# Performance work log

Hardware: AMD Instinct MI355X
Metric: run time of the kernel (lower is better)

## Reference

```python
import jax, jax.numpy as jnp
import numpy as np

ITER_N = 5  # Newton-Schulz iterations (SqrtmLayer(cov, 5))


def covpool(x):
    # x: [B, C, M]. MPNCOV CovpoolLayer: x @ I_hat @ x^T with
    # I_hat = (1/M)(I - J/M), a projector, so cov = xc @ xc^T / M.
    M = x.shape[-1]
    xc = x - x.mean(axis=-1, keepdims=True)
    return jnp.einsum('bcm,bdm->bcd', xc, xc) / M


def sqrtm_ns(A, iter_n=ITER_N):
    # MPNCOV SqrtmLayer: trace-normalized Newton-Schulz matrix square root.
    C = A.shape[-1]
    I = jnp.eye(C, dtype=A.dtype)
    normA = jnp.trace(A, axis1=-2, axis2=-1)[:, None, None]  # [B,1,1]
    Y = A / normA
    Z = jnp.broadcast_to(I, A.shape)
    for i in range(iter_n):
        T = 0.5 * (3.0 * I - Z @ Y)
        Y_new = Y @ T
        if i < iter_n - 1:
            Z = T @ Z
        Y = Y_new
    return Y * jnp.sqrt(normA)


def setup_inputs() -> dict:
    key = jax.random.key(0)
    k1, k2, k3 = jax.random.split(key, 3)
    B, C, H, W = 32, 256, 64, 64
    r = 8
    x = jax.random.normal(k1, (B, C, H, W), dtype=jnp.float32)
    w1 = jax.random.normal(k2, (C // r, C), dtype=jnp.float32) * 0.05
    b1 = jnp.zeros((C // r,), dtype=jnp.float32)
    w2 = jax.random.normal(k3, (C, C // r), dtype=jnp.float32) * 0.05
    b2 = jnp.zeros((C,), dtype=jnp.float32)
    return {'x': x, 'w1': w1, 'b1': b1, 'w2': w2, 'b2': b2}


def reference(x, w1, b1, w2, b2):
    B, C, h, w = x.shape
    # h, w < 1000 => x_sub = x (no center crop)
    xf = x.reshape(B, C, h * w)
    cov = covpool(xf)                      # [B, C, C]
    cov_sqrt = sqrtm_ns(cov, ITER_N)       # [B, C, C]
    v = cov_sqrt.mean(axis=1)              # mean over dim 1 -> [B, C]
    # 1x1 convs on a 1x1 map == dense layers
    hdn = jax.nn.relu(jnp.einsum('oc,bc->bo', w1, v) + b1)
    a = jax.nn.sigmoid(jnp.einsum('oc,bc->bo', w2, hdn) + b2)  # [B, C]
    return a[:, :, None, None] * x
```

## Files before the change

kernel.cpp:

```cpp
#include <hip/hip_runtime.h>
#include <hip/hip_bf16.h>

typedef unsigned int uint32;
using short8 = __attribute__((ext_vector_type(8))) short;
using f32x4  = __attribute__((ext_vector_type(4))) float;

#define B_ 32
#define C_ 256
#define M_ 4096

__device__ inline ushort f2bf(float f) {
  uint32 u = __builtin_bit_cast(uint32, f);
  u += 0x7FFFu + ((u >> 16) & 1u);
  return (ushort)(u >> 16);
}

__global__ __launch_bounds__(256)
void covpool_kernel(const float* __restrict__ x,
                    float* __restrict__ p0, float* __restrict__ p1,
                    float* __restrict__ p2, float* __restrict__ p3,
                    float* __restrict__ rs) {
  const int bid0 = blockIdx.x;
  const int bid  = (bid0 & 7) * 64 + (bid0 >> 3);
  const int b    = bid >> 4;
  const int tile = (bid >> 2) & 3;
  const int s    = bid & 3;
  const int rb   = (tile >> 1) * 128;
  const int cb   = (tile & 1) * 128;
  const int kb   = s * 1024;
  float* P = (s == 0) ? p0 : (s == 1) ? p1 : (s == 2) ? p2 : p3;

  const float* Xr = x + (size_t)b * C_ * M_ + (size_t)rb * M_;
  const float* Xc = x + (size_t)b * C_ * M_ + (size_t)cb * M_;

  __shared__ ushort As[128 * 64];
  __shared__ ushort Bs[128 * 64];

  const int t    = threadIdx.x;
  const int lane = t & 63;
  const int wid  = t >> 6;
  const int wr   = wid >> 1, wc = wid & 1;
  const int r0   = t >> 3;
  const int c8   = t & 7;

  float sA[4] = {0.f, 0.f, 0.f, 0.f};
  f32x4 acc[4][4];
#pragma unroll
  for (int m = 0; m < 4; ++m)
#pragma unroll
    for (int n = 0; n < 4; ++n) acc[m][n] = f32x4{0.f, 0.f, 0.f, 0.f};

  for (int k0 = kb; k0 < kb + 1024; k0 += 64) {
    __syncthreads();
#pragma unroll
    for (int i = 0; i < 4; ++i) {
      const int row = r0 + 32 * i;
      const int swz = (c8 * 16) ^ ((row & 7) << 4);
      {
        const float4 a0 = *(const float4*)(Xr + (size_t)row * M_ + k0 + c8 * 8);
        const float4 a1 = *(const float4*)(Xr + (size_t)row * M_ + k0 + c8 * 8 + 4);
        sA[i] += a0.x + a0.y + a0.z + a0.w + a1.x + a1.y + a1.z + a1.w;
        short8 h;
        h[0] = (short)f2bf(a0.x); h[1] = (short)f2bf(a0.y);
        h[2] = (short)f2bf(a0.z); h[3] = (short)f2bf(a0.w);
        h[4] = (short)f2bf(a1.x); h[5] = (short)f2bf(a1.y);
        h[6] = (short)f2bf(a1.z); h[7] = (short)f2bf(a1.w);
        *(short8*)((char*)As + row * 128 + swz) = h;
      }
      {
        const float4 b0 = *(const float4*)(Xc + (size_t)row * M_ + k0 + c8 * 8);
        const float4 b1 = *(const float4*)(Xc + (size_t)row * M_ + k0 + c8 * 8 + 4);
        short8 g;
        g[0] = (short)f2bf(b0.x); g[1] = (short)f2bf(b0.y);
        g[2] = (short)f2bf(b0.z); g[3] = (short)f2bf(b0.w);
        g[4] = (short)f2bf(b1.x); g[5] = (short)f2bf(b1.y);
        g[6] = (short)f2bf(b1.z); g[7] = (short)f2bf(b1.w);
        *(short8*)((char*)Bs + row * 128 + swz) = g;
      }
    }
    __syncthreads();
#pragma unroll
    for (int kk = 0; kk < 2; ++kk) {
      short8 af[4], bfr[4];
      const int slot = kk * 4 + (lane >> 4);
#pragma unroll
      for (int m = 0; m < 4; ++m) {
        const int ar = wr * 64 + m * 16 + (lane & 15);
        af[m] = *(const short8*)((const char*)As + ar * 128 + ((slot * 16) ^ ((ar & 7) << 4)));
      }
#pragma unroll
      for (int n = 0; n < 4; ++n) {
        const int br = wc * 64 + n * 16 + (lane & 15);
        bfr[n] = *(const short8*)((const char*)Bs + br * 128 + ((slot * 16) ^ ((br & 7) << 4)));
      }
#pragma unroll
      for (int m = 0; m < 4; ++m)
#pragma unroll
        for (int n = 0; n < 4; ++n)
          acc[m][n] = __builtin_amdgcn_mfma_f32_16x16x32_bf16(af[m], bfr[n], acc[m][n], 0, 0, 0);
    }
  }

#pragma unroll
  for (int i = 0; i < 4; ++i) {
    float v = sA[i];
    v += __shfl_xor(v, 1); v += __shfl_xor(v, 2); v += __shfl_xor(v, 4);
    if ((lane & 7) == 0) rs[b * 1024 + s * 256 + rb + r0 + 32 * i] = v;
  }

  float* Po = P + ((size_t)b << 16);
#pragma unroll
  for (int m = 0; m < 4; ++m)
#pragma unroll
    for (int n = 0; n < 4; ++n)
#pragma unroll
      for (int r = 0; r < 4; ++r) {
        const int lr = wr * 64 + m * 16 + ((lane >> 4) * 4) + r;
        const int lc = wc * 64 + n * 16 + (lane & 15);
        Po[(size_t)(rb + lr) * C_ + (cb + lc)] = acc[m][n][r];
      }
}

__global__ __launch_bounds__(256)
void reduce_kernel(const float* __restrict__ p0, const float* __restrict__ p1,
                   const float* __restrict__ p2, const float* __restrict__ p3,
                   const float* __restrict__ rs, float* __restrict__ cov) {
  const int idx = blockIdx.x * 256 + threadIdx.x;
  const int b   = idx >> 14;
  const int rem = idx & 16383;
  const int i   = rem >> 6;
  const int j4  = (rem & 63) * 4;
  const float invM = 1.0f / (float)M_;

  const float4 g0 = ((const float4*)p0)[idx];
  const float4 g1 = ((const float4*)p1)[idx];
  const float4 g2 = ((const float4*)p2)[idx];
  const float4 g3 = ((const float4*)p3)[idx];

  const float* rb_ = rs + b * 1024;
  const float mi = (rb_[i] + rb_[256 + i] + rb_[512 + i] + rb_[768 + i]) * invM;
  const float4 s0 = *(const float4*)(rb_ + j4);
  const float4 s1 = *(const float4*)(rb_ + 256 + j4);
  const float4 s2 = *(const float4*)(rb_ + 512 + j4);
  const float4 s3 = *(const float4*)(rb_ + 768 + j4);

  float4 o;
  o.x = (g0.x + g1.x + g2.x + g3.x) * invM - mi * ((s0.x + s1.x + s2.x + s3.x) * invM);
  o.y = (g0.y + g1.y + g2.y + g3.y) * invM - mi * ((s0.y + s1.y + s2.y + s3.y) * invM);
  o.z = (g0.z + g1.z + g2.z + g3.z) * invM - mi * ((s0.z + s1.z + s2.z + s3.z) * invM);
  o.w = (g0.w + g1.w + g2.w + g3.w) * invM - mi * ((s0.w + s1.w + s2.w + s3.w) * invM);
  ((float4*)cov)[idx] = o;
}

__global__ __launch_bounds__(256)
void trace_kernel(const float* __restrict__ cov, float* __restrict__ invn,
                  float* __restrict__ sqrtn) {
  const int b = blockIdx.x;
  const int t = threadIdx.x;
  float v = cov[((size_t)b << 16) + (size_t)t * 257];
#pragma unroll
  for (int o = 32; o > 0; o >>= 1) v += __shfl_xor(v, o);
  __shared__ float wsum[4];
  if ((t & 63) == 0) wsum[t >> 6] = v;
  __syncthreads();
  if (t == 0) {
    const float n = wsum[0] + wsum[1] + wsum[2] + wsum[3];
    invn[b]  = 1.0f / n;
    sqrtn[b] = sqrtf(n);
  }
}

__global__ __launch_bounds__(256)
void prep_kernel(const float* __restrict__ cov, const float* __restrict__ invn,
                 float* __restrict__ Y, float* __restrict__ Z) {
  const int idx = blockIdx.x * 256 + threadIdx.x;
  const int b  = idx >> 14;
  const int w4 = idx & 16383;
  const int i  = w4 >> 6;
  const int j  = (w4 & 63) * 4;
  const float in = invn[b];
  const float4 c = ((const float4*)cov)[idx];
  float4 y = { c.x * in, c.y * in, c.z * in, c.w * in };
  float4 z = { (j + 0 == i ? 1.5f : 0.f) - 0.5f * y.x,
               (j + 1 == i ? 1.5f : 0.f) - 0.5f * y.y,
               (j + 2 == i ? 1.5f : 0.f) - 0.5f * y.z,
               (j + 3 == i ? 1.5f : 0.f) - 0.5f * y.w };
  ((float4*)Y)[idx] = y;
  ((float4*)Z)[idx] = z;
}

#define MODE_T 0
#define MODE_W 1
#define MODE_I0 2

template <int MODE>
__global__ __launch_bounds__(256)
void gemm_ns(const float* __restrict__ A0, const float* __restrict__ A1,
             const float* __restrict__ Bm,
             float* __restrict__ O0, float* __restrict__ O1) {
  int bid = blockIdx.x;
  const float* Aall = A0;
  float* Oall = O0;
  if (MODE == MODE_W && bid >= 512) { bid -= 512; Aall = A1; Oall = O1; }
  const int b    = bid >> 4;
  const int tile = bid & 15;
  const int rb   = (tile >> 2) * 64;
  const int cb   = (tile & 3) * 64;
  const float* Ap = Aall + ((size_t)b << 16) + rb * C_;
  const float* Bp = Bm   + ((size_t)b << 16) + cb * C_;
  float* Op = Oall + ((size_t)b << 16);

  __shared__ ushort As[64 * 64];
  __shared__ ushort Bs[64 * 64];

  const int t    = threadIdx.x;
  const int lane = t & 63;
  const int wid  = t >> 6;
  const int wr   = wid >> 1, wc = wid & 1;
  const int r0   = t >> 3;
  const int c8   = t & 7;

  f32x4 acc[2][2];
#pragma unroll
  for (int m = 0; m < 2; ++m)
#pragma unroll
    for (int n = 0; n < 2; ++n) acc[m][n] = f32x4{0.f, 0.f, 0.f, 0.f};

#pragma unroll 1
  for (int k0 = 0; k0 < C_; k0 += 64) {
    __syncthreads();
#pragma unroll
    for (int i = 0; i < 2; ++i) {
      const int row = r0 + 32 * i;
      const int swz = (c8 * 16) ^ ((row & 7) << 4);
      {
        const float4 a0 = *(const float4*)(Ap + row * C_ + k0 + c8 * 8);
        const float4 a1 = *(const float4*)(Ap + row * C_ + k0 + c8 * 8 + 4);
        short8 h;
        h[0] = (short)f2bf(a0.x); h[1] = (short)f2bf(a0.y);
        h[2] = (short)f2bf(a0.z); h[3] = (short)f2bf(a0.w);
        h[4] = (short)f2bf(a1.x); h[5] = (short)f2bf(a1.y);
        h[6] = (short)f2bf(a1.z); h[7] = (short)f2bf(a1.w);
        *(short8*)((char*)As + row * 128 + swz) = h;
      }
      {
        const float4 b0 = *(const float4*)(Bp + row * C_ + k0 + c8 * 8);
        const float4 b1 = *(const float4*)(Bp + row * C_ + k0 + c8 * 8 + 4);
        short8 g;
        g[0] = (short)f2bf(b0.x); g[1] = (short)f2bf(b0.y);
        g[2] = (short)f2bf(b0.z); g[3] = (short)f2bf(b0.w);
        g[4] = (short)f2bf(b1.x); g[5] = (short)f2bf(b1.y);
        g[6] = (short)f2bf(b1.z); g[7] = (short)f2bf(b1.w);
        *(short8*)((char*)Bs + row * 128 + swz) = g;
      }
    }
    __syncthreads();
#pragma unroll
    for (int kk = 0; kk < 2; ++kk) {
      short8 af[2], bfr[2];
      const int slot = kk * 4 + (lane >> 4);
#pragma unroll
      for (int m = 0; m < 2; ++m) {
        const int ar = wr * 32 + m * 16 + (lane & 15);
        af[m] = *(const short8*)((const char*)As + ar * 128 + ((slot * 16) ^ ((ar & 7) << 4)));
      }
#pragma unroll
      for (int n = 0; n < 2; ++n) {
        const int br = wc * 32 + n * 16 + (lane & 15);
        bfr[n] = *(const short8*)((const char*)Bs + br * 128 + ((slot * 16) ^ ((br & 7) << 4)));
      }
#pragma unroll
      for (int m = 0; m < 2; ++m)
#pragma unroll
        for (int n = 0; n < 2; ++n)
          acc[m][n] = __builtin_amdgcn_mfma_f32_16x16x32_bf16(af[m], bfr[n], acc[m][n], 0, 0, 0);
    }
  }

#pragma unroll
  for (int m = 0; m < 2; ++m)
#pragma unroll
    for (int n = 0; n < 2; ++n)
#pragma unroll
      for (int r = 0; r < 4; ++r) {
        const int lr = wr * 32 + m * 16 + ((lane >> 4) * 4) + r;
        const int lc = wc * 32 + n * 16 + (lane & 15);
        const float v = acc[m][n][r];
        float o;
        if (MODE == MODE_T)       o = (((rb + lr) == (cb + lc)) ? 1.5f : 0.0f) - 0.5f * v;
        else if (MODE == MODE_W)  o = v;
        else         o = 1.5f * Ap[lr * C_ + (cb + lc)] - 0.5f * v;
        Op[(size_t)(rb + lr) * C_ + (cb + lc)] = o;
      }
}

__global__ __launch_bounds__(256)
void final_kernel(const float* __restrict__ Y, const float* __restrict__ T,
                  const float* __restrict__ sqrtn,
                  const float* __restrict__ w1, const float* __restrict__ b1,
                  const float* __restrict__ w2, const float* __restrict__ b2,
                  float* __restrict__ a) {
  const int b = blockIdx.x;
  const int c = threadIdx.x;
  __shared__ float u[C_], vv[C_], h[32];
  const float* Yb = Y + ((size_t)b << 16);
  const float* Tb = T + ((size_t)b << 16);

  float s = 0.f;
  for (int i = 0; i < C_; ++i) s += Yb[(size_t)i * C_ + c];
  u[c] = s * (1.0f / (float)C_);
  __syncthreads();

  float acc = 0.f;
  for (int k = 0; k < C_; ++k) acc += u[k] * Tb[(size_t)k * C_ + c];
  vv[c] = acc * sqrtn[b];
  __syncthreads();

  if (c < 32) {
    float hh = b1[c];
    for (int k = 0; k < C_; ++k) hh += w1[c * C_ + k] * vv[k];
    h[c] = fmaxf(hh, 0.0f);
  }
  __syncthreads();

  float aa = b2[c];
#pragma unroll
  for (int o = 0; o < 32; ++o) aa += w2[c * 32 + o] * h[o];
  a[b * C_ + c] = 1.0f / (1.0f + expf(-aa));
}

__global__ __launch_bounds__(256)
void scale_kernel(const float* __restrict__ x, const float* __restrict__ a,
                  float* __restrict__ out) {
  const int stride = gridDim.x * blockDim.x;
  const int n4 = B_ * C_ * M_ / 4;
  for (int i = blockIdx.x * blockDim.x + threadIdx.x; i < n4; i += stride) {
    const float4 v = ((const float4*)x)[i];
    const float s = a[i >> 10];
    float4 o = { v.x * s, v.y * s, v.z * s, v.w * s };
    ((float4*)out)[i] = o;
  }
}

extern "C" void kernel_launch(void* const* d_in, const int* in_sizes, int n_in,
                              void* d_out, int out_size, void* d_ws, size_t ws_size,
                              hipStream_t stream) {
  const float* x  = (const float*)d_in[0];
  const float* w1 = (const float*)d_in[1];
  const float* b1 = (const float*)d_in[2];
  const float* w2 = (const float*)d_in[3];
  const float* b2 = (const float*)d_in[4];
  float* out = (float*)d_out;

  float* ws = (float*)d_ws;
  const size_t MAT = (size_t)B_ * C_ * C_;
  float* covT = ws;
  float* YA   = ws + 1 * MAT;
  float* YB   = ws + 2 * MAT;
  float* ZA   = ws + 3 * MAT;
  float* ZB   = ws + 4 * MAT;
  float* invn  = ws + 5 * MAT;
  float* sqrtn = invn + 32;
  float* a     = sqrtn + 32;
  float* rs    = a + 32 * 256;

  covpool_kernel<<<512, 256, 0, stream>>>(x, YA, YB, ZA, ZB, rs);
  reduce_kernel<<<2048, 256, 0, stream>>>(YA, YB, ZA, ZB, rs, covT);
  trace_kernel<<<32, 256, 0, stream>>>(covT, invn, sqrtn);
  prep_kernel<<<2048, 256, 0, stream>>>(covT, invn, YA, ZA);

  gemm_ns<MODE_I0><<<512, 256, 0, stream>>>(YA, nullptr, YA, YB, nullptr);
  gemm_ns<MODE_T><<<512, 256, 0, stream>>>(ZA, nullptr, YB, covT, nullptr);
  gemm_ns<MODE_W><<<1024, 256, 0, stream>>>(YB, ZA, covT, YA, ZB);
  gemm_ns<MODE_T><<<512, 256, 0, stream>>>(ZB, nullptr, YA, covT, nullptr);
  gemm_ns<MODE_W><<<1024, 256, 0, stream>>>(YA, ZB, covT, YB, ZA);
  gemm_ns<MODE_T><<<512, 256, 0, stream>>>(ZA, nullptr, YB, covT, nullptr);
  gemm_ns<MODE_W><<<1024, 256, 0, stream>>>(YB, ZA, covT, YA, ZB);
  gemm_ns<MODE_T><<<512, 256, 0, stream>>>(ZB, nullptr, YA, covT, nullptr);

  final_kernel<<<32, 256, 0, stream>>>(YA, covT, sqrtn, w1, b1, w2, b2, a);
  scale_kernel<<<4096, 256, 0, stream>>>(x, a, out);
}
```

Before: 420.5 us.

## Store Newton-Schulz matrices in bf16, use direct-to-LDS loads, restructure covpool

Covpool now has one 1024-thread block per (batch, K-split) that computes the full 256x256 Gram from a single shared tile. This halves the global reads of x, since rows and columns come from the same data. The K split grows to 8 partial buffers, and the reduce and prep kernels are fused into one that writes bf16 Y and Z; the trace is taken directly from the partial diagonals. All Newton-Schulz intermediates are kept in bf16, and the GEMM loads use global_load_lds with swizzled addresses, cutting memory traffic and per-element conversion. The risk is lower precision from rounding intermediates to bf16 between iterations, plus more partial-buffer traffic in the reduce step.

```diff
diff --git a/kernel.cpp b/kernel.cpp
--- a/kernel.cpp
+++ b/kernel.cpp
@@ -3,81 +3,79 @@
 
 typedef unsigned int uint32;
 using short8 = __attribute__((ext_vector_type(8))) short;
+using ushort4_t = __attribute__((ext_vector_type(4))) unsigned short;
 using f32x4  = __attribute__((ext_vector_type(4))) float;
 
 #define B_ 32
 #define C_ 256
 #define M_ 4096
+#define MATF 2097152
+
+#define AS1 __attribute__((address_space(1)))
+#define AS3 __attribute__((address_space(3)))
 
 __device__ inline ushort f2bf(float f) {
   uint32 u = __builtin_bit_cast(uint32, f);
   u += 0x7FFFu + ((u >> 16) & 1u);
   return (ushort)(u >> 16);
 }
-
-__global__ __launch_bounds__(256)
-void covpool_kernel(const float* __restrict__ x,
-                    float* __restrict__ p0, float* __restrict__ p1,
-                    float* __restrict__ p2, float* __restrict__ p3,
+__device__ inline float bf2f(ushort u) {
+  uint32 v = ((uint32)u) << 16;
+  return __builtin_bit_cast(float, v);
+}
+__device__ inline void gl_lds16(const ushort* g, ushort* l) {
+  __builtin_amdgcn_global_load_lds((const AS1 void*)g, (AS3 void*)l, 16, 0, 0);
+}
+
+__global__ __launch_bounds__(1024)
+void covpool_kernel(const float* __restrict__ x, float* __restrict__ parts,
                     float* __restrict__ rs) {
-  const int bid0 = blockIdx.x;
-  const int bid  = (bid0 & 7) * 64 + (bid0 >> 3);
-  const int b    = bid >> 4;
-  const int tile = (bid >> 2) & 3;
-  const int s    = bid & 3;
-  const int rb   = (tile >> 1) * 128;
-  const int cb   = (tile & 1) * 128;
-  const int kb   = s * 1024;
-  float* P = (s == 0) ? p0 : (s == 1) ? p1 : (s == 2) ? p2 : p3;
-
-  const float* Xr = x + (size_t)b * C_ * M_ + (size_t)rb * M_;
-  const float* Xc = x + (size_t)b * C_ * M_ + (size_t)cb * M_;
-
-  __shared__ ushort As[128 * 64];
-  __shared__ ushort Bs[128 * 64];
+  const int bid = blockIdx.x;
+  const int b = bid >> 3, s = bid & 7;
+  const int kb = s * 512;
+  const float* Xb = x + (size_t)b * C_ * M_;
+  float* P = parts + (size_t)s * MATF + ((size_t)b << 16);
+
+  __shared__ ushort As[256 * 64];
 
   const int t    = threadIdx.x;
   const int lane = t & 63;
-  const int wid  = t >> 6;
-  const int wr   = wid >> 1, wc = wid & 1;
-  const int r0   = t >> 3;
-  const int c8   = t & 7;
-
-  float sA[4] = {0.f, 0.f, 0.f, 0.f};
+  const int w    = t >> 6;
+  const int wr   = w >> 2, wc = w & 3;
+  const int row  = t >> 2;
+  const int ch   = t & 3;
+
+  float rsum = 0.f;
   f32x4 acc[4][4];
 #pragma unroll
   for (int m = 0; m < 4; ++m)
 #pragma unroll
     for (int n = 0; n < 4; ++n) acc[m][n] = f32x4{0.f, 0.f, 0.f, 0.f};
 
-  for (int k0 = kb; k0 < kb + 1024; k0 += 64) {
+  const int swzbase = (row & 7) << 4;
+  char* wbase = (char*)As + row * 128;
+
+  for (int k0 = kb; k0 < kb + 512; k0 += 64) {
     __syncthreads();
-#pragma unroll
-    for (int i = 0; i < 4; ++i) {
-      const int row = r0 + 32 * i;
-      const int swz = (c8 * 16) ^ ((row & 7) << 4);
-      {
-        const float4 a0 = *(const float4*)(Xr + (size_t)row * M_ + k0 + c8 * 8);
-        const float4 a1 = *(const float4*)(Xr + (size_t)row * M_ + k0 + c8 * 8 + 4);
-        sA[i] += a0.x + a0.y + a0.z + a0.w + a1.x + a1.y + a1.z + a1.w;
-        short8 h;
-        h[0] = (short)f2bf(a0.x); h[1] = (short)f2bf(a0.y);
-        h[2] = (short)f2bf(a0.z); h[3] = (short)f2bf(a0.w);
-        h[4] = (short)f2bf(a1.x); h[5] = (short)f2bf(a1.y);
-        h[6] = (short)f2bf(a1.z); h[7] = (short)f2bf(a1.w);
-        *(short8*)((char*)As + row * 128 + swz) = h;
-      }
-      {
-        const float4 b0 = *(const float4*)(Xc + (size_t)row * M_ + k0 + c8 * 8);
-        const float4 b1 = *(const float4*)(Xc + (size_t)row * M_ + k0 + c8 * 8 + 4);
-        short8 g;
-        g[0] = (short)f2bf(b0.x); g[1] = (short)f2bf(b0.y);
-        g[2] = (short)f2bf(b0.z); g[3] = (short)f2bf(b0.w);
-        g[4] = (short)f2bf(b1.x); g[5] = (short)f2bf(b1.y);
-        g[6] = (short)f2bf(b1.z); g[7] = (short)f2bf(b1.w);
-        *(short8*)((char*)Bs + row * 128 + swz) = g;
-      }
-    }
+    const float* src = Xb + (size_t)row * M_ + k0 + ch * 16;
+    const float4 v0 = ((const float4*)src)[0];
+    const float4 v1 = ((const float4*)src)[1];
+    const float4 v2 = ((const float4*)src)[2];
+    const float4 v3 = ((const float4*)src)[3];
+    rsum += v0.x + v0.y + v0.z + v0.w + v1.x + v1.y + v1.z + v1.w +
+            v2.x + v2.y + v2.z + v2.w + v3.x + v3.y + v3.z + v3.w;
+    short8 h0, h1;
+    h0[0] = (short)f2bf(v0.x); h0[1] = (short)f2bf(v0.y);
+    h0[2] = (short)f2bf(v0.z); h0[3] = (short)f2bf(v0.w);
+    h0[4] = (short)f2bf(v1.x); h0[5] = (short)f2bf(v1.y);
+    h0[6] = (short)f2bf(v1.z); h0[7] = (short)f2bf(v1.w);
+    h1[0] = (short)f2bf(v2.x); h1[1] = (short)f2bf(v2.y);
+    h1[2] = (short)f2bf(v2.z); h1[3] = (short)f2bf(v2.w);
+    h1[4] = (short)f2bf(v3.x); h1[5] = (short)f2bf(v3.y);
+    h1[6] = (short)f2bf(v3.z); h1[7] = (short)f2bf(v3.w);
+    const int c0 = ch * 2;
+    *(short8*)(wbase + ((c0 * 16) ^ swzbase))       = h0;
+    *(short8*)(wbase + (((c0 + 1) * 16) ^ swzbase)) = h1;
     __syncthreads();
 #pragma unroll
     for (int kk = 0; kk < 2; ++kk) {
@@ -91,7 +89,7 @@
 #pragma unroll
       for (int n = 0; n < 4; ++n) {
         const int br = wc * 64 + n * 16 + (lane & 15);
-        bfr[n] = *(const short8*)((const char*)Bs + br * 128 + ((slot * 16) ^ ((br & 7) << 4)));
+        bfr[n] = *(const short8*)((const char*)As + br * 128 + ((slot * 16) ^ ((br & 7) << 4)));
       }
 #pragma unroll
       for (int m = 0; m < 4; ++m)
@@ -101,14 +99,10 @@
     }
   }
 
-#pragma unroll
-  for (int i = 0; i < 4; ++i) {
-    float v = sA[i];
-    v += __shfl_xor(v, 1); v += __shfl_xor(v, 2); v += __shfl_xor(v, 4);
-    if ((lane & 7) == 0) rs[b * 1024 + s * 256 + rb + r0 + 32 * i] = v;
-  }
-
-  float* Po = P + ((size_t)b << 16);
+  rsum += __shfl_xor(rsum, 1);
+  rsum += __shfl_xor(rsum, 2);
+  if (ch == 0) rs[b * 2048 + s * 256 + row] = rsum;
+
 #pragma unroll
   for (int m = 0; m < 4; ++m)
 #pragma unroll
@@ -117,76 +111,75 @@
       for (int r = 0; r < 4; ++r) {
         const int lr = wr * 64 + m * 16 + ((lane >> 4) * 4) + r;
         const int lc = wc * 64 + n * 16 + (lane & 15);
-        Po[(size_t)(rb + lr) * C_ + (cb + lc)] = acc[m][n][r];
-      }
-}
-
-__global__ __launch_bounds__(256)
-void reduce_kernel(const float* __restrict__ p0, const float* __restrict__ p1,
-                   const float* __restrict__ p2, const float* __restrict__ p3,
-                   const float* __restrict__ rs, float* __restrict__ cov) {
+        P[(size_t)lr * C_ + lc] = acc[m][n][r];
+      }
+}
+
+__global__ __launch_bounds__(256)
+void trace_kernel(const float* __restrict__ parts, const float* __restrict__ rs,
+                  float* __restrict__ invn, float* __restrict__ sqrtn) {
+  const int b = blockIdx.x;
+  const int i = threadIdx.x;
+  const float invM = 1.0f / (float)M_;
+  float d = 0.f, m = 0.f;
+#pragma unroll
+  for (int s = 0; s < 8; ++s) {
+    d += parts[(size_t)s * MATF + ((size_t)b << 16) + (size_t)i * 257];
+    m += rs[b * 2048 + s * 256 + i];
+  }
+  const float mu = m * invM;
+  float v = d * invM - mu * mu;
+#pragma unroll
+  for (int o = 32; o > 0; o >>= 1) v += __shfl_xor(v, o);
+  __shared__ float wsum[4];
+  if ((i & 63) == 0) wsum[i >> 6] = v;
+  __syncthreads();
+  if (i == 0) {
+    const float n = wsum[0] + wsum[1] + wsum[2] + wsum[3];
+    invn[b]  = 1.0f / n;
+    sqrtn[b] = sqrtf(n);
+  }
+}
+
+__global__ __launch_bounds__(256)
+void reduceprep_kernel(const float* __restrict__ parts, const float* __restrict__ rs,
+                       const float* __restrict__ invn,
+                       ushort* __restrict__ Y0, ushort* __restrict__ Z1) {
   const int idx = blockIdx.x * 256 + threadIdx.x;
   const int b   = idx >> 14;
   const int rem = idx & 16383;
   const int i   = rem >> 6;
-  const int j4  = (rem & 63) * 4;
+  const int j   = (rem & 63) * 4;
   const float invM = 1.0f / (float)M_;
-
-  const float4 g0 = ((const float4*)p0)[idx];
-  const float4 g1 = ((const float4*)p1)[idx];
-  const float4 g2 = ((const float4*)p2)[idx];
-  const float4 g3 = ((const float4*)p3)[idx];
-
-  const float* rb_ = rs + b * 1024;
-  const float mi = (rb_[i] + rb_[256 + i] + rb_[512 + i] + rb_[768 + i]) * invM;
-  const float4 s0 = *(const float4*)(rb_ + j4);
-  const float4 s1 = *(const float4*)(rb_ + 256 + j4);
-  const float4 s2 = *(const float4*)(rb_ + 512 + j4);
-  const float4 s3 = *(const float4*)(rb_ + 768 + j4);
-
-  float4 o;
-  o.x = (g0.x + g1.x + g2.x + g3.x) * invM - mi * ((s0.x + s1.x + s2.x + s3.x) * invM);
-  o.y = (g0.y + g1.y + g2.y + g3.y) * invM - mi * ((s0.y + s1.y + s2.y + s3.y) * invM);
-  o.z = (g0.z + g1.z + g2.z + g3.z) * invM - mi * ((s0.z + s1.z + s2.z + s3.z) * invM);
-  o.w = (g0.w + g1.w + g2.w + g3.w) * invM - mi * ((s0.w + s1.w + s2.w + s3.w) * invM);
-  ((float4*)cov)[idx] = o;
-}
-
-__global__ __launch_bounds__(256)
-void trace_kernel(const float* __restrict__ cov, float* __restrict__ invn,
-                  float* __restrict__ sqrtn) {
-  const int b = blockIdx.x;
-  const int t = threadIdx.x;
-  float v = cov[((size_t)b << 16) + (size_t)t * 257];
-#pragma unroll
-  for (int o = 32; o > 0; o >>= 1) v += __shfl_xor(v, o);
-  __shared__ float wsum[4];
-  if ((t & 63) == 0) wsum[t >> 6] = v;
-  __syncthreads();
-  if (t == 0) {
-    const float n = wsum[0] + wsum[1] + wsum[2] + wsum[3];
-    invn[b]  = 1.0f / n;
-    sqrtn[b] = sqrtf(n);
-  }
-}
-
-__global__ __launch_bounds__(256)
-void prep_kernel(const float* __restrict__ cov, const float* __restrict__ invn,
-                 float* __restrict__ Y, float* __restrict__ Z) {
-  const int idx = blockIdx.x * 256 + threadIdx.x;
-  const int b  = idx >> 14;
-  const int w4 = idx & 16383;
-  const int i  = w4 >> 6;
-  const int j  = (w4 & 63) * 4;
+  const float4* p4 = (const float4*)parts;
+
+  float4 g = {0.f, 0.f, 0.f, 0.f};
+  float  mi = 0.f;
+  float4 mj = {0.f, 0.f, 0.f, 0.f};
+#pragma unroll
+  for (int s = 0; s < 8; ++s) {
+    const float4 gs = p4[(size_t)s * (MATF / 4) + idx];
+    g.x += gs.x; g.y += gs.y; g.z += gs.z; g.w += gs.w;
+    const float* rrow = rs + b * 2048 + s * 256;
+    mi += rrow[i];
+    const float4 ms = *(const float4*)(rrow + j);
+    mj.x += ms.x; mj.y += ms.y; mj.z += ms.z; mj.w += ms.w;
+  }
+  mi *= invM;
   const float in = invn[b];
-  const float4 c = ((const float4*)cov)[idx];
-  float4 y = { c.x * in, c.y * in, c.z * in, c.w * in };
-  float4 z = { (j + 0 == i ? 1.5f : 0.f) - 0.5f * y.x,
-               (j + 1 == i ? 1.5f : 0.f) - 0.5f * y.y,
-               (j + 2 == i ? 1.5f : 0.f) - 0.5f * y.z,
-               (j + 3 == i ? 1.5f : 0.f) - 0.5f * y.w };
-  ((float4*)Y)[idx] = y;
-  ((float4*)Z)[idx] = z;
+  float y0 = (g.x * invM - mi * (mj.x * invM)) * in;
+  float y1 = (g.y * invM - mi * (mj.y * invM)) * in;
+  float y2 = (g.z * invM - mi * (mj.z * invM)) * in;
+  float y3 = (g.w * invM - mi * (mj.w * invM)) * in;
+
+  ushort4_t yv, zv;
+  yv[0] = f2bf(y0); yv[1] = f2bf(y1); yv[2] = f2bf(y2); yv[3] = f2bf(y3);
+  zv[0] = f2bf((j + 0 == i ? 1.5f : 0.f) - 0.5f * y0);
+  zv[1] = f2bf((j + 1 == i ? 1.5f : 0.f) - 0.5f * y1);
+  zv[2] = f2bf((j + 2 == i ? 1.5f : 0.f) - 0.5f * y2);
+  zv[3] = f2bf((j + 3 == i ? 1.5f : 0.f) - 0.5f * y3);
+  ((ushort4_t*)Y0)[idx] = yv;
+  ((ushort4_t*)Z1)[idx] = zv;
 }
 
 #define MODE_T 0
@@ -195,20 +188,22 @@
 
 template <int MODE>
 __global__ __launch_bounds__(256)
-void gemm_ns(const float* __restrict__ A0, const float* __restrict__ A1,
-             const float* __restrict__ Bm,
-             float* __restrict__ O0, float* __restrict__ O1) {
-  int bid = blockIdx.x;
-  const float* Aall = A0;
-  float* Oall = O0;
+void gemm_ns(const ushort* __restrict__ A0, const ushort* __restrict__ A1,
+             const ushort* __restrict__ Bm,
+             ushort* __restrict__ O0, ushort* __restrict__ O1) {
+  const int bid0 = blockIdx.x;
+  int bid = (MODE == MODE_W) ? ((bid0 & 7) * 128 + (bid0 >> 3))
+                             : ((bid0 & 7) * 64 + (bid0 >> 3));
+  const ushort* Aall = A0;
+  ushort* Oall = O0;
   if (MODE == MODE_W && bid >= 512) { bid -= 512; Aall = A1; Oall = O1; }
   const int b    = bid >> 4;
   const int tile = bid & 15;
   const int rb   = (tile >> 2) * 64;
   const int cb   = (tile & 3) * 64;
-  const float* Ap = Aall + ((size_t)b << 16) + rb * C_;
-  const float* Bp = Bm   + ((size_t)b << 16) + cb * C_;
-  float* Op = Oall + ((size_t)b << 16);
+  const ushort* Ap = Aall + ((size_t)b << 16) + rb * C_;
+  const ushort* Bp = Bm   + ((size_t)b << 16) + cb * C_;
+  ushort* Op = Oall + ((size_t)b << 16);
 
   __shared__ ushort As[64 * 64];
   __shared__ ushort Bs[64 * 64];
@@ -217,8 +212,11 @@
   const int lane = t & 63;
   const int wid  = t >> 6;
   const int wr   = wid >> 1, wc = wid & 1;
-  const int r0   = t >> 3;
-  const int c8   = t & 7;
+
+  const int srow0 = t >> 3;
+  const int sc0   = (t & 7) ^ (srow0 & 7);
+  const int srow1 = 32 + srow0;
+  const int sc1   = (t & 7) ^ (srow1 & 7);
 
   f32x4 acc[2][2];
 #pragma unroll
@@ -226,34 +224,12 @@
 #pragma unroll
     for (int n = 0; n < 2; ++n) acc[m][n] = f32x4{0.f, 0.f, 0.f, 0.f};
 
-#pragma unroll 1
   for (int k0 = 0; k0 < C_; k0 += 64) {
     __syncthreads();
-#pragma unroll
-    for (int i = 0; i < 2; ++i) {
-      const int row = r0 + 32 * i;
-      const int swz = (c8 * 16) ^ ((row & 7) << 4);
-      {
-        const float4 a0 = *(const float4*)(Ap + row * C_ + k0 + c8 * 8);
-        const float4 a1 = *(const float4*)(Ap + row * C_ + k0 + c8 * 8 + 4);
-        short8 h;
-        h[0] = (short)f2bf(a0.x); h[1] = (short)f2bf(a0.y);
-        h[2] = (short)f2bf(a0.z); h[3] = (short)f2bf(a0.w);
-        h[4] = (short)f2bf(a1.x); h[5] = (short)f2bf(a1.y);
-        h[6] = (short)f2bf(a1.z); h[7] = (short)f2bf(a1.w);
-        *(short8*)((char*)As + row * 128 + swz) = h;
-      }
-      {
-        const float4 b0 = *(const float4*)(Bp + row * C_ + k0 + c8 * 8);
-        const float4 b1 = *(const float4*)(Bp + row * C_ + k0 + c8 * 8 + 4);
-        short8 g;
-        g[0] = (short)f2bf(b0.x); g[1] = (short)f2bf(b0.y);
-        g[2] = (short)f2bf(b0.z); g[3] = (short)f2bf(b0.w);
-        g[4] = (short)f2bf(b1.x); g[5] = (short)f2bf(b1.y);
-        g[6] = (short)f2bf(b1.z); g[7] = (short)f2bf(b1.w);
-        *(short8*)((char*)Bs + row * 128 + swz) = g;
-      }
-    }
+    gl_lds16(Ap + (size_t)srow0 * C_ + k0 + sc0 * 8, (ushort*)((char*)As + wid * 1024));
+    gl_lds16(Ap + (size_t)srow1 * C_ + k0 + sc1 * 8, (ushort*)((char*)As + 4096 + wid * 1024));
+    gl_lds16(Bp + (size_t)srow0 * C_ + k0 + sc0 * 8, (ushort*)((char*)Bs + wid * 1024));
+    gl_lds16(Bp + (size_t)srow1 * C_ + k0 + sc1 * 8, (ushort*)((char*)Bs + 4096 + wid * 1024));
     __syncthreads();
 #pragma unroll
     for (int kk = 0; kk < 2; ++kk) {
@@ -289,13 +265,13 @@
         float o;
         if (MODE == MODE_T)       o = (((rb + lr) == (cb + lc)) ? 1.5f : 0.0f) - 0.5f * v;
         else if (MODE == MODE_W)  o = v;
-        else         o = 1.5f * Ap[lr * C_ + (cb + lc)] - 0.5f * v;
-        Op[(size_t)(rb + lr) * C_ + (cb + lc)] = o;
-      }
-}
-
-__global__ __launch_bounds__(256)
-void final_kernel(const float* __restrict__ Y, const float* __restrict__ T,
+        else         o = 1.5f * bf2f(Ap[lr * C_ + (cb + lc)]) - 0.5f * v;
+        Op[(size_t)(rb + lr) * C_ + (cb + lc)] = f2bf(o);
+      }
+}
+
+__global__ __launch_bounds__(256)
+void final_kernel(const ushort* __restrict__ Y, const ushort* __restrict__ T,
                   const float* __restrict__ sqrtn,
                   const float* __restrict__ w1, const float* __restrict__ b1,
                   const float* __restrict__ w2, const float* __restrict__ b2,
@@ -303,16 +279,16 @@
   const int b = blockIdx.x;
   const int c = threadIdx.x;
   __shared__ float u[C_], vv[C_], h[32];
-  const float* Yb = Y + ((size_t)b << 16);
-  const float* Tb = T + ((size_t)b << 16);
+  const ushort* Yb = Y + ((size_t)b << 16);
+  const ushort* Tb = T + ((size_t)b << 16);
 
   float s = 0.f;
-  for (int i = 0; i < C_; ++i) s += Yb[(size_t)i * C_ + c];
+  for (int i = 0; i < C_; ++i) s += bf2f(Yb[(size_t)i * C_ + c]);
   u[c] = s * (1.0f / (float)C_);
   __syncthreads();
 
   float acc = 0.f;
-  for (int k = 0; k < C_; ++k) acc += u[k] * Tb[(size_t)k * C_ + c];
+  for (int k = 0; k < C_; ++k) acc += u[k] * bf2f(Tb[(size_t)k * C_ + c]);
   vv[c] = acc * sqrtn[b];
   __syncthreads();
 
@@ -353,31 +329,31 @@
   float* out = (float*)d_out;
 
   float* ws = (float*)d_ws;
-  const size_t MAT = (size_t)B_ * C_ * C_;
-  float* covT = ws;
-  float* YA   = ws + 1 * MAT;
-  float* YB   = ws + 2 * MAT;
-  float* ZA   = ws + 3 * MAT;
-  float* ZB   = ws + 4 * MAT;
-  float* invn  = ws + 5 * MAT;
+  float* parts = ws;
+  float* rs    = ws + 8 * (size_t)MATF;
+  float* invn  = rs + 65536;
   float* sqrtn = invn + 32;
   float* a     = sqrtn + 32;
-  float* rs    = a + 32 * 256;
-
-  covpool_kernel<<<512, 256, 0, stream>>>(x, YA, YB, ZA, ZB, rs);
-  reduce_kernel<<<2048, 256, 0, stream>>>(YA, YB, ZA, ZB, rs, covT);
-  trace_kernel<<<32, 256, 0, stream>>>(covT, invn, sqrtn);
-  prep_kernel<<<2048, 256, 0, stream>>>(covT, invn, YA, ZA);
-
-  gemm_ns<MODE_I0><<<512, 256, 0, stream>>>(YA, nullptr, YA, YB, nullptr);
-  gemm_ns<MODE_T><<<512, 256, 0, stream>>>(ZA, nullptr, YB, covT, nullptr);
-  gemm_ns<MODE_W><<<1024, 256, 0, stream>>>(YB, ZA, covT, YA, ZB);
-  gemm_ns<MODE_T><<<512, 256, 0, stream>>>(ZB, nullptr, YA, covT, nullptr);
-  gemm_ns<MODE_W><<<1024, 256, 0, stream>>>(YA, ZB, covT, YB, ZA);
-  gemm_ns<MODE_T><<<512, 256, 0, stream>>>(ZA, nullptr, YB, covT, nullptr);
-  gemm_ns<MODE_W><<<1024, 256, 0, stream>>>(YB, ZA, covT, YA, ZB);
-  gemm_ns<MODE_T><<<512, 256, 0, stream>>>(ZB, nullptr, YA, covT, nullptr);
-
-  final_kernel<<<32, 256, 0, stream>>>(YA, covT, sqrtn, w1, b1, w2, b2, a);
+  ushort* bfb  = (ushort*)(a + 8192);
+  ushort* Yb0  = bfb;
+  ushort* Yb1  = bfb + 1 * (size_t)MATF;
+  ushort* Zb0  = bfb + 2 * (size_t)MATF;
+  ushort* Zb1  = bfb + 3 * (size_t)MATF;
+  ushort* Tb   = bfb + 4 * (size_t)MATF;
+
+  covpool_kernel<<<256, 1024, 0, stream>>>(x, parts, rs);
+  trace_kernel<<<32, 256, 0, stream>>>(parts, rs, invn, sqrtn);
+  reduceprep_kernel<<<2048, 256, 0, stream>>>(parts, rs, invn, Yb0, Zb0);
+
+  gemm_ns<MODE_I0><<<512, 256, 0, stream>>>(Yb0, nullptr, Yb0, Yb1, nullptr);
+  gemm_ns<MODE_T><<<512, 256, 0, stream>>>(Zb0, nullptr, Yb1, Tb, nullptr);
+  gemm_ns<MODE_W><<<1024, 256, 0, stream>>>(Yb1, Zb0, Tb, Yb0, Zb1);
+  gemm_ns<MODE_T><<<512, 256, 0, stream>>>(Zb1, nullptr, Yb0, Tb, nullptr);
+  gemm_ns<MODE_W><<<1024, 256, 0, stream>>>(Yb0, Zb1, Tb, Yb1, Zb0);
+  gemm_ns<MODE_T><<<512, 256, 0, stream>>>(Zb0, nullptr, Yb1, Tb, nullptr);
+  gemm_ns<MODE_W><<<1024, 256, 0, stream>>>(Yb1, Zb0, Tb, Yb0, Zb1);
+  gemm_ns<MODE_T><<<512, 256, 0, stream>>>(Zb1, nullptr, Yb0, Tb, nullptr);
+
+  final_kernel<<<32, 256, 0, stream>>>(Yb0, Tb, sqrtn, w1, b1, w2, b2, a);
   scale_kernel<<<4096, 256, 0, stream>>>(x, a, out);
 }
```

After: 367.9 us. 1.14x faster.
